# Kernel optimization log

Hardware: AMD Instinct MI355X
Metric: run time of the kernel (lower is better)

The kernel has to match this reference:

```python
import jax, jax.numpy as jnp
import numpy as np

N_NODES = 50000
N_EDGES = 800000
IN_FEATS = 256
HID = 128          # total hidden width
HEADS = 4
HEAD_DIM = HID // HEADS  # 32
OUT_FEATS = 64
NEG_SLOPE = 0.2    # DGL GATConv default


def setup_inputs() -> dict:
    key = jax.random.key(0)
    ks = jax.random.split(key, 16)
    feat = jax.random.normal(ks[0], (N_NODES, IN_FEATS), dtype=jnp.float32)
    src = jax.random.randint(ks[1], (N_EDGES,), 0, N_NODES, dtype=jnp.int64)
    dst = jax.random.randint(ks[2], (N_EDGES,), 0, N_NODES, dtype=jnp.int64)

    def glorot(k, shape):
        fan_in, fan_out = shape[0], shape[-1] if len(shape) > 1 else shape[0]
        s = jnp.sqrt(2.0 / (fan_in + fan_out)).astype(jnp.float32)
        return jax.random.normal(k, shape, dtype=jnp.float32) * s

    # layer 0: in 256 -> 4 heads x 32
    W1 = glorot(ks[3], (IN_FEATS, HEADS * HEAD_DIM))
    al1 = glorot(ks[4], (HEADS, HEAD_DIM)) * 0.1
    ar1 = glorot(ks[5], (HEADS, HEAD_DIM)) * 0.1
    b1 = jnp.zeros((HEADS * HEAD_DIM,), dtype=jnp.float32)
    # layer 1: 128 -> 4 heads x 32
    W2 = glorot(ks[6], (HID, HEADS * HEAD_DIM))
    al2 = glorot(ks[7], (HEADS, HEAD_DIM)) * 0.1
    ar2 = glorot(ks[8], (HEADS, HEAD_DIM)) * 0.1
    b2 = jnp.zeros((HEADS * HEAD_DIM,), dtype=jnp.float32)
    # layer 2: 128 -> 1 head x 64
    W3 = glorot(ks[9], (HID, OUT_FEATS))
    al3 = glorot(ks[10], (1, OUT_FEATS)) * 0.1
    ar3 = glorot(ks[11], (1, OUT_FEATS)) * 0.1
    b3 = jnp.zeros((OUT_FEATS,), dtype=jnp.float32)

    return {"feat": feat, "src": src, "dst": dst,
            "W1": W1, "al1": al1, "ar1": ar1, "b1": b1,
            "W2": W2, "al2": al2, "ar2": ar2, "b2": b2,
            "W3": W3, "al3": al3, "ar3": ar3, "b3": b3}


def gat_layer(x, src, dst, W, al, ar, b, heads, head_dim):
    # x: [N, F_in] -> h: [N, H, D]
    n = x.shape[0]
    h = (x @ W).reshape(n, heads, head_dim)
    el = jnp.sum(h * al, axis=-1)  # [N, H]
    er = jnp.sum(h * ar, axis=-1)  # [N, H]
    e = jax.nn.leaky_relu(el[src] + er[dst], NEG_SLOPE)  # [E, H]
    # segment softmax over incoming edges of each dst node
    m = jax.ops.segment_max(e, dst, num_segments=n)      # [N, H]
    ex = jnp.exp(e - m[dst])                              # [E, H]
    denom = jax.ops.segment_sum(ex, dst, num_segments=n)  # [N, H]
    alpha = ex / denom[dst]                               # [E, H]
    msg = alpha[:, :, None] * h[src]                      # [E, H, D]
    out = jax.ops.segment_sum(msg, dst, num_segments=n)   # [N, H, D]
    return out + b.reshape(1, heads, head_dim)


def reference(feat, src, dst, W1, al1, ar1, b1, W2, al2, ar2, b2, W3, al3, ar3, b3):
    # dropout is identity (inference mode) for a deterministic reference
    h = gat_layer(feat, src, dst, W1, al1, ar1, b1, HEADS, HEAD_DIM)
    h = jax.nn.relu(h).reshape(N_NODES, -1)  # flatten(1)
    h = gat_layer(h, src, dst, W2, al2, ar2, b2, HEADS, HEAD_DIM)
    h = jax.nn.relu(h).reshape(N_NODES, -1)
    h = gat_layer(h, src, dst, W3, al3, ar3, b3, 1, OUT_FEATS)
    return h.reshape(N_NODES, -1)  # [N, out_feats]
```

## Files before the change

### kernel.cpp

```cpp
#include <hip/hip_runtime.h>
#include <hip/hip_fp16.h>
#include <cfloat>

#define N_NODES 50000
#define N_EDGES 800000
#define NBUK 196
#define NAB 512
#define EPB 1563

typedef _Float16 half8 __attribute__((ext_vector_type(8)));
typedef float f32x4 __attribute__((ext_vector_type(4)));

__global__ void wtrans_all(const float* __restrict__ W1, const float* __restrict__ W2,
                           const float* __restrict__ W3, __half* __restrict__ wt1,
                           __half* __restrict__ wt2, __half* __restrict__ wt3) {
    int i = blockIdx.x * blockDim.x + threadIdx.x;
    if (i < 32768) {
        int n = i / 256, k = i % 256;
        wt1[i] = __float2half(W1[k * 128 + n]);
    } else if (i < 32768 + 16384) {
        int j = i - 32768;
        int n = j / 128, k = j % 128;
        wt2[j] = __float2half(W2[k * 128 + n]);
    } else if (i < 32768 + 16384 + 8192) {
        int j = i - 32768 - 16384;
        int n = j / 128, k = j % 128;
        wt3[j] = __float2half(W3[k * 64 + n]);
    }
}

template <int BN, int K, bool AF32>
__global__ __launch_bounds__(256)
void gemm_mfma(const void* __restrict__ xin, const __half* __restrict__ wt,
               __half* __restrict__ hh, const float* __restrict__ al,
               const float* __restrict__ ar, float* __restrict__ el,
               float* __restrict__ er) {
    constexpr int BM = 64, BK = 64;
    constexpr int LDA = BK + 8;
    constexpr int NT = BN / 16;
    constexpr int NH = (BN == 128) ? 4 : 1;
    constexpr int TPH = NT / NH;
    __shared__ __align__(16) _Float16 As[BM][LDA];
    __shared__ __align__(16) _Float16 Bs[BN][LDA];

    const __half* xh = (const __half*)xin;
    const float*  xf = (const float*)xin;

    const int t    = threadIdx.x;
    const int lane = t & 63;
    const int w    = t >> 6;
    const int r0   = blockIdx.x * BM;
    const int l15  = lane & 15;
    const int g    = lane >> 4;

    f32x4 acc[NT];
#pragma unroll
    for (int ct = 0; ct < NT; ++ct) acc[ct] = (f32x4){0.f, 0.f, 0.f, 0.f};

    const int arow = t >> 2;
    const int aseg = t & 3;
    const bool aok = (r0 + arow) < N_NODES;
    const int brow = t >> 1;
    const int bseg = t & 1;

    for (int k0 = 0; k0 < K; k0 += BK) {
#pragma unroll
        for (int s = 0; s < 2; ++s) {
            int seg = aseg + 4 * s;
            uint4 v = make_uint4(0, 0, 0, 0);
            if constexpr (AF32) {
                if (aok) {
                    const float* p = xf + (long long)(r0 + arow) * K + k0 + seg * 8;
                    float4 f0 = *reinterpret_cast<const float4*>(p);
                    float4 f1 = *reinterpret_cast<const float4*>(p + 4);
                    union { uint4 u; __half2 h[4]; } cv;
                    cv.h[0] = __floats2half2_rn(f0.x, f0.y);
                    cv.h[1] = __floats2half2_rn(f0.z, f0.w);
                    cv.h[2] = __floats2half2_rn(f1.x, f1.y);
                    cv.h[3] = __floats2half2_rn(f1.z, f1.w);
                    v = cv.u;
                }
            } else {
                if (aok) v = *reinterpret_cast<const uint4*>(xh + (long long)(r0 + arow) * K + k0 + seg * 8);
            }
            *reinterpret_cast<uint4*>(&As[arow][seg * 8]) = v;
        }
        if (brow < BN) {
#pragma unroll
            for (int s = 0; s < 4; ++s) {
                int seg = bseg + 2 * s;
                uint4 v = *reinterpret_cast<const uint4*>(wt + (long long)brow * K + k0 + seg * 8);
                *reinterpret_cast<uint4*>(&Bs[brow][seg * 8]) = v;
            }
        }
        __syncthreads();

#pragma unroll
        for (int kb = 0; kb < 2; ++kb) {
            half8 a = *reinterpret_cast<const half8*>(&As[w * 16 + l15][kb * 32 + g * 8]);
#pragma unroll
            for (int ct = 0; ct < NT; ++ct) {
                half8 b = *reinterpret_cast<const half8*>(&Bs[ct * 16 + l15][kb * 32 + g * 8]);
                acc[ct] = __builtin_amdgcn_mfma_f32_16x16x32_f16(a, b, acc[ct], 0, 0, 0);
            }
        }
        __syncthreads();
    }

    float alv[NT], arv[NT];
#pragma unroll
    for (int ct = 0; ct < NT; ++ct) {
        alv[ct] = al[ct * 16 + l15];
        arv[ct] = ar[ct * 16 + l15];
    }

    float pel[NH][4], per_[NH][4];
#pragma unroll
    for (int hd = 0; hd < NH; ++hd)
#pragma unroll
        for (int b = 0; b < 4; ++b) { pel[hd][b] = 0.f; per_[hd][b] = 0.f; }

#pragma unroll
    for (int ct = 0; ct < NT; ++ct) {
        int hd = ct / TPH;
#pragma unroll
        for (int b = 0; b < 4; ++b) {
            pel[hd][b] += acc[ct][b] * alv[ct];
            per_[hd][b] += acc[ct][b] * arv[ct];
        }
    }
#pragma unroll
    for (int off = 1; off < 16; off <<= 1) {
#pragma unroll
        for (int hd = 0; hd < NH; ++hd)
#pragma unroll
            for (int b = 0; b < 4; ++b) {
                pel[hd][b] += __shfl_xor(pel[hd][b], off);
                per_[hd][b] += __shfl_xor(per_[hd][b], off);
            }
    }

#pragma unroll
    for (int b = 0; b < 4; ++b) {
        int row = r0 + w * 16 + g * 4 + b;
        if (row >= N_NODES) continue;
#pragma unroll
        for (int ct = 0; ct < NT; ++ct)
            hh[(long long)row * BN + ct * 16 + l15] = __float2half(acc[ct][b]);
        if (l15 == 0) {
#pragma unroll
            for (int hd = 0; hd < NH; ++hd) {
                el[row * NH + hd] = pel[hd][b];
                er[row * NH + hd] = per_[hd][b];
            }
        }
    }
}

__global__ void zero_counts(int* __restrict__ counts) {
    int i = blockIdx.x * blockDim.x + threadIdx.x;
    if (i < N_NODES) counts[i] = 0;
}

__global__ void hist_kernel(const int* __restrict__ dst, int* __restrict__ counts) {
    int e = blockIdx.x * blockDim.x + threadIdx.x;
    if (e < N_EDGES) atomicAdd(counts + dst[e], 1);
}

__global__ __launch_bounds__(1024)
void scan_local(const int* __restrict__ counts, int* __restrict__ row_ptr,
                int* __restrict__ bsum) {
    __shared__ int wsums[16];
    const int tid = threadIdx.x, lane = tid & 63, wid = tid >> 6;
    const int i = blockIdx.x * 1024 + tid;
    int v = (i < N_NODES) ? counts[i] : 0;
    int incl = v;
#pragma unroll
    for (int off = 1; off < 64; off <<= 1) {
        int t = __shfl_up(incl, off);
        if (lane >= off) incl += t;
    }
    if (lane == 63) wsums[wid] = incl;
    __syncthreads();
    if (wid == 0) {
        int ws = (lane < 16) ? wsums[lane] : 0;
#pragma unroll
        for (int off = 1; off < 16; off <<= 1) {
            int t = __shfl_up(ws, off);
            if (lane >= off) ws += t;
        }
        if (lane < 16) wsums[lane] = ws;
        if (lane == 15) bsum[blockIdx.x] = ws;
    }
    __syncthreads();
    int woff = (wid > 0) ? wsums[wid - 1] : 0;
    if (i < N_NODES) row_ptr[i] = woff + incl - v;
}

__global__ void scan_bsums(int* __restrict__ bsum, int* __restrict__ row_ptr, int nb) {
    const int lane = threadIdx.x;
    int v = (lane < nb) ? bsum[lane] : 0;
    int incl = v;
#pragma unroll
    for (int off = 1; off < 64; off <<= 1) {
        int t = __shfl_up(incl, off);
        if (lane >= off) incl += t;
    }
    if (lane < nb) bsum[lane] = incl - v;
    if (lane == 63) row_ptr[N_NODES] = incl;
}

__global__ void scan_add(int* __restrict__ row_ptr, const int* __restrict__ bsum) {
    int i = blockIdx.x * blockDim.x + threadIdx.x;
    if (i < N_NODES) row_ptr[i] += bsum[i >> 10];
}

__global__ __launch_bounds__(256)
void part_hist(const int* __restrict__ dst, int* __restrict__ pbh) {
    __shared__ int cnt[NBUK];
    for (int i = threadIdx.x; i < NBUK; i += 256) cnt[i] = 0;
    __syncthreads();
    const int e0 = blockIdx.x * EPB, e1 = min(N_EDGES, e0 + EPB);
    for (int e = e0 + threadIdx.x; e < e1; e += 256)
        atomicAdd(&cnt[dst[e] >> 8], 1);
    __syncthreads();
    for (int i = threadIdx.x; i < NBUK; i += 256)
        pbh[i * NAB + blockIdx.x] = cnt[i];
}

__global__ __launch_bounds__(512)
void part_scan(const int* __restrict__ row_ptr, int* __restrict__ pbh) {
    __shared__ int wsums[8];
    const int b = blockIdx.x, t = threadIdx.x, lane = t & 63, wid = t >> 6;
    int v = pbh[b * NAB + t];
    int incl = v;
#pragma unroll
    for (int off = 1; off < 64; off <<= 1) {
        int s = __shfl_up(incl, off);
        if (lane >= off) incl += s;
    }
    if (lane == 63) wsums[wid] = incl;
    __syncthreads();
    if (wid == 0) {
        int ws = (lane < 8) ? wsums[lane] : 0;
#pragma unroll
        for (int off = 1; off < 8; off <<= 1) {
            int s = __shfl_up(ws, off);
            if (lane >= off) ws += s;
        }
        if (lane < 8) wsums[lane] = ws;
    }
    __syncthreads();
    int woff = (wid > 0) ? wsums[wid - 1] : 0;
    pbh[b * NAB + t] = row_ptr[b * 256] + woff + incl - v;
}

__global__ __launch_bounds__(256)
void part_scatter(const int* __restrict__ src, const int* __restrict__ dst,
                  const int* __restrict__ pbh, unsigned* __restrict__ binned) {
    __shared__ int cur[NBUK];
    for (int i = threadIdx.x; i < NBUK; i += 256)
        cur[i] = pbh[i * NAB + blockIdx.x];
    __syncthreads();
    const int e0 = blockIdx.x * EPB, e1 = min(N_EDGES, e0 + EPB);
    for (int e = e0 + threadIdx.x; e < e1; e += 256) {
        int d = dst[e];
        int pos = atomicAdd(&cur[d >> 8], 1);
        binned[pos] = ((unsigned)src[e] << 8) | (unsigned)(d & 255);
    }
}

__global__ __launch_bounds__(256)
void part_fin(const int* __restrict__ row_ptr, const unsigned* __restrict__ binned,
              int* __restrict__ sorted_src) {
    __shared__ int cur[256];
    const int b  = blockIdx.x;
    const int n0 = b * 256;
    const int n1 = min(N_NODES, n0 + 256);
    const int t  = threadIdx.x;
    if (n0 + t < n1) cur[t] = row_ptr[n0 + t];
    __syncthreads();
    const int e0 = row_ptr[n0], e1 = row_ptr[n1];
    for (int e = e0 + t; e < e1; e += 256) {
        unsigned p = binned[e];
        int pos = atomicAdd(&cur[p & 255u], 1);
        sorted_src[pos] = (int)(p >> 8);
    }
}

__global__ __launch_bounds__(256)
void gat_agg_h4(const int* __restrict__ row_ptr, const int* __restrict__ sorted_src,
                const float* __restrict__ el, const float* __restrict__ er,
                const __half* __restrict__ hh, const float* __restrict__ bias,
                __half* __restrict__ out) {
    const uint4* hh16 = reinterpret_cast<const uint4*>(hh);
    const int lane = threadIdx.x & 63;
    const int wid  = threadIdx.x >> 6;
    const int n    = blockIdx.x * 4 + wid;
    if (n >= N_NODES) return;

    const int start = row_ptr[n];
    const int deg   = row_ptr[n + 1] - start;

    const float4 ern = *reinterpret_cast<const float4*>(er + n * 4);

    const int ho = lane >> 4;
    const float eoa = (ho & 2) ? ern.z : ern.x;
    const float eob = (ho & 2) ? ern.w : ern.y;
    const float ero = (ho & 1) ? eob : eoa;

    const int q   = lane >> 4;
    const int cg  = lane & 15;
    const int hr  = cg >> 2;
    const int hsh = hr << 4;

    float a[8];
#pragma unroll
    for (int i = 0; i < 8; ++i) a[i] = 0.f;
    float ssum = 0.f;

    for (int base = 0; base < deg; base += 64) {
        int cnt = min(64, deg - base);
        int sr = 0;
        if (lane < cnt) sr = sorted_src[start + base + lane];

        float w[4];
#pragma unroll
        for (int k = 0; k < 4; ++k) {
            int ee = (lane & 15) + 16 * k;
            int sk = __shfl(sr, ee);
            float v = el[sk * 4 + ho] + ero;
            v = (v >= 0.f) ? v : 0.2f * v;
            w[k] = (ee < cnt) ? __expf(v) : 0.f;
        }

#pragma unroll
        for (int k = 0; k < 4; ++k) {
            int rem = cnt - 16 * k;
            if (rem > 0) {
                int quads = (min(rem, 16) + 3) >> 2;
#pragma unroll 4
                for (int it = 0; it < quads; ++it) {
                    int e0 = 16 * k + 4 * it + q;
                    int   se = __shfl(sr, e0);
                    float we = __shfl(w[k], (4 * it + q) | hsh);
                    uint4 raw = hh16[(long long)se * 16 + cg];
                    union { uint4 u; __half2 h[4]; } cv; cv.u = raw;
                    float2 v0 = __half22float2(cv.h[0]);
                    float2 v1 = __half22float2(cv.h[1]);
                    float2 v2 = __half22float2(cv.h[2]);
                    float2 v3 = __half22float2(cv.h[3]);
                    a[0] += we * v0.x; a[1] += we * v0.y;
                    a[2] += we * v1.x; a[3] += we * v1.y;
                    a[4] += we * v2.x; a[5] += we * v2.y;
                    a[6] += we * v3.x; a[7] += we * v3.y;
                    ssum += we;
                }
            }
        }
    }

#pragma unroll
    for (int i = 0; i < 8; ++i) {
        a[i] += __shfl_xor(a[i], 16);
        a[i] += __shfl_xor(a[i], 32);
    }
    ssum += __shfl_xor(ssum, 16);
    ssum += __shfl_xor(ssum, 32);

    if (lane < 16) {
        float inv = (ssum > 0.f) ? 1.f / ssum : 0.f;
        int c0 = cg * 8;
        float4 b0 = *reinterpret_cast<const float4*>(bias + c0);
        float4 b1 = *reinterpret_cast<const float4*>(bias + c0 + 4);
        float o0 = fmaxf(a[0] * inv + b0.x, 0.f);
        float o1 = fmaxf(a[1] * inv + b0.y, 0.f);
        float o2 = fmaxf(a[2] * inv + b0.z, 0.f);
        float o3 = fmaxf(a[3] * inv + b0.w, 0.f);
        float o4 = fmaxf(a[4] * inv + b1.x, 0.f);
        float o5 = fmaxf(a[5] * inv + b1.y, 0.f);
        float o6 = fmaxf(a[6] * inv + b1.z, 0.f);
        float o7 = fmaxf(a[7] * inv + b1.w, 0.f);
        union { uint4 u; __half2 h[4]; } pk;
        pk.h[0] = __floats2half2_rn(o0, o1);
        pk.h[1] = __floats2half2_rn(o2, o3);
        pk.h[2] = __floats2half2_rn(o4, o5);
        pk.h[3] = __floats2half2_rn(o6, o7);
        *reinterpret_cast<uint4*>(out + (long long)n * 128 + c0) = pk.u;
    }
}

__global__ __launch_bounds__(256)
void gat_agg_h1(const int* __restrict__ row_ptr, const int* __restrict__ sorted_src,
                const float* __restrict__ el, const float* __restrict__ er,
                const __half* __restrict__ hh, const float* __restrict__ bias,
                float* __restrict__ out) {
    const uint4* hh16 = reinterpret_cast<const uint4*>(hh);
    const int lane = threadIdx.x & 63;
    const int wid  = threadIdx.x >> 6;
    const int n    = blockIdx.x * 4 + wid;
    if (n >= N_NODES) return;

    const int start = row_ptr[n];
    const int deg   = row_ptr[n + 1] - start;
    const float ern = er[n];

    const int q  = lane >> 3;
    const int cg = lane & 7;

    float a[8];
#pragma unroll
    for (int i = 0; i < 8; ++i) a[i] = 0.f;
    float ssum = 0.f;

    for (int base = 0; base < deg; base += 64) {
        int cnt = min(64, deg - base);
        int sr = 0;
        float w = 0.f;
        if (lane < cnt) {
            sr = sorted_src[start + base + lane];
            float v = el[sr] + ern;
            v = (v >= 0.f) ? v : 0.2f * v;
            w = __expf(v);
        }
        int octs = (cnt + 7) >> 3;
#pragma unroll 2
        for (int it = 0; it < octs; ++it) {
            int e0 = 8 * it + q;
            int   se = __shfl(sr, e0);
            float we = __shfl(w, e0);
            uint4 raw = hh16[(long long)se * 8 + cg];
            union { uint4 u; __half2 h[4]; } cv; cv.u = raw;
            float2 v0 = __half22float2(cv.h[0]);
            float2 v1 = __half22float2(cv.h[1]);
            float2 v2 = __half22float2(cv.h[2]);
            float2 v3 = __half22float2(cv.h[3]);
            a[0] += we * v0.x; a[1] += we * v0.y;
            a[2] += we * v1.x; a[3] += we * v1.y;
            a[4] += we * v2.x; a[5] += we * v2.y;
            a[6] += we * v3.x; a[7] += we * v3.y;
            ssum += we;
        }
    }

#pragma unroll
    for (int i = 0; i < 8; ++i) {
        a[i] += __shfl_xor(a[i], 8);
        a[i] += __shfl_xor(a[i], 16);
        a[i] += __shfl_xor(a[i], 32);
    }
    ssum += __shfl_xor(ssum, 8);
    ssum += __shfl_xor(ssum, 16);
    ssum += __shfl_xor(ssum, 32);

    if (lane < 8) {
        float inv = (ssum > 0.f) ? 1.f / ssum : 0.f;
        int c0 = cg * 8;
        float4 b0 = *reinterpret_cast<const float4*>(bias + c0);
        float4 b1 = *reinterpret_cast<const float4*>(bias + c0 + 4);
        float4 oA = make_float4(a[0] * inv + b0.x, a[1] * inv + b0.y,
                                a[2] * inv + b0.z, a[3] * inv + b0.w);
        float4 oB = make_float4(a[4] * inv + b1.x, a[5] * inv + b1.y,
                                a[6] * inv + b1.z, a[7] * inv + b1.w);
        *reinterpret_cast<float4*>(out + (long long)n * 64 + c0)     = oA;
        *reinterpret_cast<float4*>(out + (long long)n * 64 + c0 + 4) = oB;
    }
}

extern "C" void kernel_launch(void* const* d_in, const int* in_sizes, int n_in,
                              void* d_out, int out_size, void* d_ws, size_t ws_size,
                              hipStream_t stream) {
    const float* feat = (const float*)d_in[0];
    const int*   src  = (const int*)d_in[1];
    const int*   dst  = (const int*)d_in[2];
    const float* W1  = (const float*)d_in[3];
    const float* al1 = (const float*)d_in[4];
    const float* ar1 = (const float*)d_in[5];
    const float* b1  = (const float*)d_in[6];
    const float* W2  = (const float*)d_in[7];
    const float* al2 = (const float*)d_in[8];
    const float* ar2 = (const float*)d_in[9];
    const float* b2  = (const float*)d_in[10];
    const float* W3  = (const float*)d_in[11];
    const float* al3 = (const float*)d_in[12];
    const float* ar3 = (const float*)d_in[13];
    const float* b3  = (const float*)d_in[14];

    float* ws = (float*)d_ws;
    __half* xh2 = (__half*)ws;
    __half* hh  = (__half*)(ws + (long long)N_NODES * 64);
    float* el   = ws + (long long)N_NODES * 128;
    float* er   = el + (long long)N_NODES * 4;
    __half* wt1 = (__half*)(er + (long long)N_NODES * 4);
    __half* wt2 = wt1 + 32768;
    __half* wt3 = wt2 + 16384;
    int* counts     = (int*)(wt3 + 8192);
    int* row_ptr    = counts  + N_NODES;
    int* pbh        = row_ptr + N_NODES + 1;
    int* bsum       = pbh + NBUK * NAB;
    int* sorted_src = bsum + 64;
    unsigned* binned = (unsigned*)(sorted_src + N_EDGES);

    const int SB = (N_NODES + 1023) / 1024;
    zero_counts<<<(N_NODES + 255) / 256, 256, 0, stream>>>(counts);
    hist_kernel<<<(N_EDGES + 255) / 256, 256, 0, stream>>>(dst, counts);
    scan_local<<<SB, 1024, 0, stream>>>(counts, row_ptr, bsum);
    scan_bsums<<<1, 64, 0, stream>>>(bsum, row_ptr, SB);
    scan_add<<<(N_NODES + 255) / 256, 256, 0, stream>>>(row_ptr, bsum);
    part_hist<<<NAB, 256, 0, stream>>>(dst, pbh);
    part_scan<<<NBUK, 512, 0, stream>>>(row_ptr, pbh);
    part_scatter<<<NAB, 256, 0, stream>>>(src, dst, pbh, binned);
    part_fin<<<NBUK, 256, 0, stream>>>(row_ptr, binned, sorted_src);

    wtrans_all<<<(57344 + 255) / 256, 256, 0, stream>>>(W1, W2, W3, wt1, wt2, wt3);

    const int gblocks = (N_NODES + 63) / 64;
    const int nblocks = (N_NODES + 3) / 4;

    gemm_mfma<128, 256, true><<<gblocks, 256, 0, stream>>>(feat, wt1, hh, al1, ar1, el, er);
    gat_agg_h4<<<nblocks, 256, 0, stream>>>(row_ptr, sorted_src, el, er, hh, b1, xh2);

    gemm_mfma<128, 128, false><<<gblocks, 256, 0, stream>>>(xh2, wt2, hh, al2, ar2, el, er);
    gat_agg_h4<<<nblocks, 256, 0, stream>>>(row_ptr, sorted_src, el, er, hh, b2, xh2);

    gemm_mfma<64, 128, false><<<gblocks, 256, 0, stream>>>(xh2, wt3, hh, al3, ar3, el, er);
    gat_agg_h1<<<nblocks, 256, 0, stream>>>(row_ptr, sorted_src, el, er, hh, b3, (float*)d_out);
}
```

Measured before the change: 230.7 us.

## Derive CSR row pointers from bucket partition instead of separate histogram and scan

Removes the per-node histogram with global atomics and its three-kernel scan. Bucket starts now come from a small scan over per-bucket totals. Each final partition block builds its local per-node counts in shared memory and writes row_ptr itself. This cuts several kernel launches and 800k global atomics, at the cost of an extra pass over the binned edges inside part_fin.

```diff
diff --git a/kernel.cpp b/kernel.cpp
--- a/kernel.cpp
+++ b/kernel.cpp
@@ -157,64 +157,6 @@
     }
 }
 
-__global__ void zero_counts(int* __restrict__ counts) {
-    int i = blockIdx.x * blockDim.x + threadIdx.x;
-    if (i < N_NODES) counts[i] = 0;
-}
-
-__global__ void hist_kernel(const int* __restrict__ dst, int* __restrict__ counts) {
-    int e = blockIdx.x * blockDim.x + threadIdx.x;
-    if (e < N_EDGES) atomicAdd(counts + dst[e], 1);
-}
-
-__global__ __launch_bounds__(1024)
-void scan_local(const int* __restrict__ counts, int* __restrict__ row_ptr,
-                int* __restrict__ bsum) {
-    __shared__ int wsums[16];
-    const int tid = threadIdx.x, lane = tid & 63, wid = tid >> 6;
-    const int i = blockIdx.x * 1024 + tid;
-    int v = (i < N_NODES) ? counts[i] : 0;
-    int incl = v;
-#pragma unroll
-    for (int off = 1; off < 64; off <<= 1) {
-        int t = __shfl_up(incl, off);
-        if (lane >= off) incl += t;
-    }
-    if (lane == 63) wsums[wid] = incl;
-    __syncthreads();
-    if (wid == 0) {
-        int ws = (lane < 16) ? wsums[lane] : 0;
-#pragma unroll
-        for (int off = 1; off < 16; off <<= 1) {
-            int t = __shfl_up(ws, off);
-            if (lane >= off) ws += t;
-        }
-        if (lane < 16) wsums[lane] = ws;
-        if (lane == 15) bsum[blockIdx.x] = ws;
-    }
-    __syncthreads();
-    int woff = (wid > 0) ? wsums[wid - 1] : 0;
-    if (i < N_NODES) row_ptr[i] = woff + incl - v;
-}
-
-__global__ void scan_bsums(int* __restrict__ bsum, int* __restrict__ row_ptr, int nb) {
-    const int lane = threadIdx.x;
-    int v = (lane < nb) ? bsum[lane] : 0;
-    int incl = v;
-#pragma unroll
-    for (int off = 1; off < 64; off <<= 1) {
-        int t = __shfl_up(incl, off);
-        if (lane >= off) incl += t;
-    }
-    if (lane < nb) bsum[lane] = incl - v;
-    if (lane == 63) row_ptr[N_NODES] = incl;
-}
-
-__global__ void scan_add(int* __restrict__ row_ptr, const int* __restrict__ bsum) {
-    int i = blockIdx.x * blockDim.x + threadIdx.x;
-    if (i < N_NODES) row_ptr[i] += bsum[i >> 10];
-}
-
 __global__ __launch_bounds__(256)
 void part_hist(const int* __restrict__ dst, int* __restrict__ pbh) {
     __shared__ int cnt[NBUK];
@@ -229,7 +171,7 @@
 }
 
 __global__ __launch_bounds__(512)
-void part_scan(const int* __restrict__ row_ptr, int* __restrict__ pbh) {
+void part_scan(int* __restrict__ pbh, int* __restrict__ btot) {
     __shared__ int wsums[8];
     const int b = blockIdx.x, t = threadIdx.x, lane = t & 63, wid = t >> 6;
     int v = pbh[b * NAB + t];
@@ -252,15 +194,46 @@
     }
     __syncthreads();
     int woff = (wid > 0) ? wsums[wid - 1] : 0;
-    pbh[b * NAB + t] = row_ptr[b * 256] + woff + incl - v;
+    int excl = woff + incl - v;
+    pbh[b * NAB + t] = excl;
+    if (t == NAB - 1) btot[b] = excl + v;
+}
+
+__global__ __launch_bounds__(256)
+void bucket_scan(const int* __restrict__ btot, int* __restrict__ bstart) {
+    __shared__ int wsums[4];
+    const int t = threadIdx.x, lane = t & 63, wid = t >> 6;
+    int v = (t < NBUK) ? btot[t] : 0;
+    int incl = v;
+#pragma unroll
+    for (int off = 1; off < 64; off <<= 1) {
+        int s = __shfl_up(incl, off);
+        if (lane >= off) incl += s;
+    }
+    if (lane == 63) wsums[wid] = incl;
+    __syncthreads();
+    if (wid == 0) {
+        int ws = (lane < 4) ? wsums[lane] : 0;
+#pragma unroll
+        for (int off = 1; off < 4; off <<= 1) {
+            int s = __shfl_up(ws, off);
+            if (lane >= off) ws += s;
+        }
+        if (lane < 4) wsums[lane] = ws;
+    }
+    __syncthreads();
+    int woff = (wid > 0) ? wsums[wid - 1] : 0;
+    if (t < NBUK) bstart[t] = woff + incl - v;
+    if (t == 0) bstart[NBUK] = N_EDGES;
 }
 
 __global__ __launch_bounds__(256)
 void part_scatter(const int* __restrict__ src, const int* __restrict__ dst,
-                  const int* __restrict__ pbh, unsigned* __restrict__ binned) {
+                  const int* __restrict__ pbh, const int* __restrict__ bstart,
+                  unsigned* __restrict__ binned) {
     __shared__ int cur[NBUK];
     for (int i = threadIdx.x; i < NBUK; i += 256)
-        cur[i] = pbh[i * NAB + blockIdx.x];
+        cur[i] = bstart[i] + pbh[i * NAB + blockIdx.x];
     __syncthreads();
     const int e0 = blockIdx.x * EPB, e1 = min(N_EDGES, e0 + EPB);
     for (int e = e0 + threadIdx.x; e < e1; e += 256) {
@@ -271,19 +244,51 @@
 }
 
 __global__ __launch_bounds__(256)
-void part_fin(const int* __restrict__ row_ptr, const unsigned* __restrict__ binned,
-              int* __restrict__ sorted_src) {
-    __shared__ int cur[256];
+void part_fin(const int* __restrict__ bstart, const unsigned* __restrict__ binned,
+              int* __restrict__ sorted_src, int* __restrict__ row_ptr) {
+    __shared__ int cnt[256];
+    __shared__ int wsums[4];
     const int b  = blockIdx.x;
     const int n0 = b * 256;
-    const int n1 = min(N_NODES, n0 + 256);
-    const int t  = threadIdx.x;
-    if (n0 + t < n1) cur[t] = row_ptr[n0 + t];
-    __syncthreads();
-    const int e0 = row_ptr[n0], e1 = row_ptr[n1];
+    const int t  = threadIdx.x, lane = t & 63, wid = t >> 6;
+    const int e0 = bstart[b], e1 = bstart[b + 1];
+
+    cnt[t] = 0;
+    __syncthreads();
+    for (int e = e0 + t; e < e1; e += 256)
+        atomicAdd(&cnt[binned[e] & 255u], 1);
+    __syncthreads();
+
+    int v = cnt[t];
+    int incl = v;
+#pragma unroll
+    for (int off = 1; off < 64; off <<= 1) {
+        int s = __shfl_up(incl, off);
+        if (lane >= off) incl += s;
+    }
+    if (lane == 63) wsums[wid] = incl;
+    __syncthreads();
+    if (wid == 0) {
+        int ws = (lane < 4) ? wsums[lane] : 0;
+#pragma unroll
+        for (int off = 1; off < 4; off <<= 1) {
+            int s = __shfl_up(ws, off);
+            if (lane >= off) ws += s;
+        }
+        if (lane < 4) wsums[lane] = ws;
+    }
+    __syncthreads();
+    int excl = ((wid > 0) ? wsums[wid - 1] : 0) + incl - v;
+
+    if (n0 + t < N_NODES) row_ptr[n0 + t] = e0 + excl;
+    if (b == NBUK - 1 && t == 0) row_ptr[N_NODES] = N_EDGES;
+
+    __syncthreads();
+    cnt[t] = e0 + excl;
+    __syncthreads();
     for (int e = e0 + t; e < e1; e += 256) {
         unsigned p = binned[e];
-        int pos = atomicAdd(&cur[p & 255u], 1);
+        int pos = atomicAdd(&cnt[p & 255u], 1);
         sorted_src[pos] = (int)(p >> 8);
     }
 }
@@ -494,23 +499,18 @@
     __half* wt1 = (__half*)(er + (long long)N_NODES * 4);
     __half* wt2 = wt1 + 32768;
     __half* wt3 = wt2 + 16384;
-    int* counts     = (int*)(wt3 + 8192);
-    int* row_ptr    = counts  + N_NODES;
+    int* row_ptr    = (int*)(wt3 + 8192);
     int* pbh        = row_ptr + N_NODES + 1;
-    int* bsum       = pbh + NBUK * NAB;
-    int* sorted_src = bsum + 64;
+    int* btot       = pbh + NBUK * NAB;
+    int* bstart     = btot + NBUK;
+    int* sorted_src = bstart + NBUK + 1;
     unsigned* binned = (unsigned*)(sorted_src + N_EDGES);
 
-    const int SB = (N_NODES + 1023) / 1024;
-    zero_counts<<<(N_NODES + 255) / 256, 256, 0, stream>>>(counts);
-    hist_kernel<<<(N_EDGES + 255) / 256, 256, 0, stream>>>(dst, counts);
-    scan_local<<<SB, 1024, 0, stream>>>(counts, row_ptr, bsum);
-    scan_bsums<<<1, 64, 0, stream>>>(bsum, row_ptr, SB);
-    scan_add<<<(N_NODES + 255) / 256, 256, 0, stream>>>(row_ptr, bsum);
     part_hist<<<NAB, 256, 0, stream>>>(dst, pbh);
-    part_scan<<<NBUK, 512, 0, stream>>>(row_ptr, pbh);
-    part_scatter<<<NAB, 256, 0, stream>>>(src, dst, pbh, binned);
-    part_fin<<<NBUK, 256, 0, stream>>>(row_ptr, binned, sorted_src);
+    part_scan<<<NBUK, 512, 0, stream>>>(pbh, btot);
+    bucket_scan<<<1, 256, 0, stream>>>(btot, bstart);
+    part_scatter<<<NAB, 256, 0, stream>>>(src, dst, pbh, bstart, binned);
+    part_fin<<<NBUK, 256, 0, stream>>>(bstart, binned, sorted_src, row_ptr);
 
     wtrans_all<<<(57344 + 255) / 256, 256, 0, stream>>>(W1, W2, W3, wt1, wt2, wt3);
 
```

New measurement: 188.8 us. 1.22x faster.
